# Performance work log

Measured on AMD Instinct MI355X. Metric: run time of the kernel, lower is better.

## Reference

```python
import jax, jax.numpy as jnp
import numpy as np

WS = 7   # window_size
SS = 3   # shift_size
NH = 6   # num_heads
EPS = 1e-5


def _partition(x, ws):
    # [b,h,w,c] -> [b*(h//ws)*(w//ws), ws*ws, c]
    b, h, w, c = x.shape
    x = x.reshape(b, h // ws, ws, w // ws, ws, c)
    return x.transpose(0, 1, 3, 2, 4, 5).reshape(-1, ws * ws, c)


def _reverse(windows, ws, h, w, b):
    c = windows.shape[-1]
    x = windows.reshape(b, h // ws, w // ws, ws, ws, c)
    return x.transpose(0, 1, 3, 2, 4, 5).reshape(b, h, w, c)


def _make_mask(h, w, ws, ss):
    # static (numpy) shifted-window attention mask, [nw, ws*ws, ws*ws]
    img = np.zeros((h, w), dtype=np.float32)
    slices = (slice(0, -ws), slice(-ws, -ss), slice(-ss, None))
    cnt = 0
    for hs in slices:
        for wsl in slices:
            img[hs, wsl] = cnt
            cnt += 1
    mw = img.reshape(h // ws, ws, w // ws, ws).transpose(0, 2, 1, 3).reshape(-1, ws * ws)
    am = mw[:, None, :] - mw[:, :, None]
    mask = np.where(am != 0, -100.0, 0.0).astype(np.float32)
    return jnp.asarray(mask)


def _layernorm(x, g, b):
    mu = jnp.mean(x, axis=-1, keepdims=True)
    var = jnp.var(x, axis=-1, keepdims=True)
    return (x - mu) * jax.lax.rsqrt(var + EPS) * g + b


def setup_inputs() -> dict:
    key = jax.random.key(0)
    ks = jax.random.split(key, 8)
    dim = 192
    s = lambda fan: 1.0 / np.sqrt(fan)
    return {
        "x": jax.random.normal(ks[0], (64, 56, 56, dim), dtype=jnp.float32),
        "n1_g": jnp.ones((dim,), jnp.float32),
        "n1_b": jnp.zeros((dim,), jnp.float32),
        "qkv_w": jax.random.normal(ks[1], (dim, 3 * dim), jnp.float32) * s(dim),
        "qkv_b": jnp.zeros((3 * dim,), jnp.float32),
        "proj_w": jax.random.normal(ks[2], (dim, dim), jnp.float32) * s(dim),
        "proj_b": jnp.zeros((dim,), jnp.float32),
        "n2_g": jnp.ones((dim,), jnp.float32),
        "n2_b": jnp.zeros((dim,), jnp.float32),
        "w1": jax.random.normal(ks[3], (dim, 4 * dim), jnp.float32) * s(dim),
        "b1": jnp.zeros((4 * dim,), jnp.float32),
        "w2": jax.random.normal(ks[4], (4 * dim, dim), jnp.float32) * s(4 * dim),
        "b2": jnp.zeros((dim,), jnp.float32),
    }


def reference(x, n1_g, n1_b, qkv_w, qkv_b, proj_w, proj_b, n2_g, n2_b, w1, b1, w2, b2):
    b, h, w, c = x.shape
    hd = c // NH
    scale = hd ** -0.5

    sc = x
    xn = _layernorm(x, n1_g, n1_b)
    sx = jnp.roll(xn, shift=(-SS, -SS), axis=(1, 2))

    xw = _partition(sx, WS)                      # [B_, n, c], n = WS*WS
    B_, n, _ = xw.shape

    qkv = xw @ qkv_w + qkv_b                      # [B_, n, 3c]
    qkv = qkv.reshape(B_, n, 3, NH, hd).transpose(2, 0, 3, 1, 4)
    q, k, v = qkv[0], qkv[1], qkv[2]              # [B_, NH, n, hd]

    attn = jnp.einsum("whnd,whmd->whnm", q, k) * scale   # [B_, NH, n, n]
    mask = _make_mask(h, w, WS, SS)               # [nw, n, n]
    nw = mask.shape[0]
    attn = attn.reshape(b // nw * 1 if False else b, nw, NH, n, n) if False else attn.reshape(B_ // nw, nw, NH, n, n)
    attn = attn + mask[None, :, None, :, :]
    attn = attn.reshape(-1, NH, n, n)
    attn = jax.nn.softmax(attn, axis=-1)

    out = jnp.einsum("whnm,whmd->whnd", attn, v)  # [B_, NH, n, hd]
    out = out.transpose(0, 2, 1, 3).reshape(B_, n, c)
    out = out @ proj_w + proj_b

    sx = _reverse(out, WS, h, w, b)
    xs = jnp.roll(sx, shift=(SS, SS), axis=(1, 2))

    x2 = sc + xs
    x2n = _layernorm(x2, n2_g, n2_b)
    mlp = jax.nn.gelu(x2n @ w1 + b1, approximate=False) @ w2 + b2
    return x2 + mlp
```

## Files before the change

kernel.cpp:

```cpp
#include <hip/hip_runtime.h>

typedef __attribute__((ext_vector_type(4))) float f32x4;
typedef __attribute__((ext_vector_type(8))) short bf16x8;
typedef __attribute__((ext_vector_type(2))) unsigned int u32x2;

#define NHEAD 6

__device__ __forceinline__ unsigned short f2bf(float f){
  union{float f;unsigned int u;}c; c.f=f;
  unsigned int x=c.u;
  return (unsigned short)((x + 0x7FFFu + ((x>>16)&1u)) >> 16);
}
__device__ __forceinline__ unsigned int cvtpk(float a, float b){
  unsigned int r;
  asm("v_cvt_pk_bf16_f32 %0, %1, %2" : "=v"(r) : "v"(a), "v"(b));
  return r;
}

__global__ void wt_kernel(const float* __restrict__ w, unsigned short* __restrict__ wt,
                          int K, int N){
  int idx = blockIdx.x*256 + threadIdx.x;
  if (idx >= K*N) return;
  int k = idx / N, n = idx - k*N;
  wt[(size_t)n*K + k] = f2bf(w[idx]);
}

template<int SHIFT>
__global__ __launch_bounds__(256) void ln_kernel(const float* __restrict__ x,
    const float* __restrict__ gw, const float* __restrict__ bw,
    unsigned short* __restrict__ out){
  int tok  = blockIdx.x*4 + (threadIdx.x>>6);
  int lane = threadIdx.x & 63;
  const float* row = x + (size_t)tok*192;
  float4 v = make_float4(0.f,0.f,0.f,0.f);
  if (lane < 48) v = *(const float4*)(row + lane*4);
  float s  = v.x+v.y+v.z+v.w;
  float s2 = v.x*v.x+v.y*v.y+v.z*v.z+v.w*v.w;
  #pragma unroll
  for (int off=32; off; off>>=1){ s += __shfl_xor(s,off); s2 += __shfl_xor(s2,off); }
  float mu = s*(1.f/192.f);
  float rs = rsqrtf(s2*(1.f/192.f) - mu*mu + 1e-5f);
  size_t otok;
  if (SHIFT){
    int b = tok/3136; int hw = tok - b*3136; int h = hw/56; int w = hw - h*56;
    int hs = h-3; if (hs<0) hs += 56;
    int wsh = w-3; if (wsh<0) wsh += 56;
    int wr = hs/7, r = hs - wr*7, wc = wsh/7, c = wsh - wc*7;
    otok = ((size_t)b*64 + wr*8 + wc)*49 + r*7 + c;
  } else {
    otok = (size_t)tok;
  }
  if (lane < 48){
    int cb = lane*4;
    float4 g4 = *(const float4*)(gw + cb);
    float4 b4 = *(const float4*)(bw + cb);
    u32x2 o;
    o.x = cvtpk((v.x-mu)*rs*g4.x + b4.x, (v.y-mu)*rs*g4.y + b4.y);
    o.y = cvtpk((v.z-mu)*rs*g4.z + b4.z, (v.w-mu)*rs*g4.w + b4.w);
    *(u32x2*)(out + otok*192 + cb) = o;
  }
}

enum { EPI_QKV=0, EPI_PROJ=1, EPI_GELU=2, EPI_FINAL=3 };

__device__ __forceinline__ float gelu_fast(float v){
  float t = v*(1.59576912f + 0.07135481f*v*v);
  float e = __expf(-t);
  return v/(1.f + e);
}

template<int EPI>
__global__ __launch_bounds__(256) void gemm_kernel(
    const unsigned short* __restrict__ A,
    const unsigned short* __restrict__ BT,
    const float* __restrict__ bias,
    const float* __restrict__ res,
    void* __restrict__ Cout,
    int M, int N, int K)
{
  __shared__ unsigned short lA[128*64];
  __shared__ unsigned short lB[64*64];
  const int tid  = threadIdx.x;
  const int wave = tid>>6, lane = tid&63;
  const int wm = wave>>1, wn = wave&1;
  const int lr = lane&15, lh = lane>>4;

  const int Nb = N>>6;
  int bid = blockIdx.x;
  int yb = bid/(8*Nb); int rr = bid - yb*8*Nb; int xq = rr>>3; int y8 = rr&7;
  const int m0 = (yb*8 + y8)*128, n0 = xq*64;

  f32x4 zero = {0.f,0.f,0.f,0.f};
  f32x4 acc[4][2];
  #pragma unroll
  for (int i=0;i<4;i++){ acc[i][0]=zero; acc[i][1]=zero; }

  const int row8 = tid>>3;
  const int sw   = row8 & 7;
  const int csw  = ((tid&7) ^ sw)*8;
  const unsigned short* Ag = A  + (size_t)(m0 + row8)*K + csw;
  const unsigned short* Bg = BT + (size_t)(n0 + row8)*K + csw;

  for (int kt=0; kt<K; kt+=64){
    __syncthreads();
    #pragma unroll
    for (int i=0;i<4;i++){
      __builtin_amdgcn_global_load_lds(
        (const __attribute__((address_space(1))) void*)(Ag + (size_t)i*32*K + kt),
        (__attribute__((address_space(3))) void*)(lA + (i*256 + wave*64)*8),
        16, 0, 0);
    }
    #pragma unroll
    for (int i=0;i<2;i++){
      __builtin_amdgcn_global_load_lds(
        (const __attribute__((address_space(1))) void*)(Bg + (size_t)i*32*K + kt),
        (__attribute__((address_space(3))) void*)(lB + (i*256 + wave*64)*8),
        16, 0, 0);
    }
    __syncthreads();

    bf16x8 af[4][2], bfv[2][2];
    #pragma unroll
    for (int mi=0;mi<4;mi++)
      #pragma unroll
      for (int ks=0;ks<2;ks++){
        int arow = wm*64+mi*16+lr;
        af[mi][ks] = *(const bf16x8*)&lA[arow*64 + (((ks*4+lh) ^ (lr&7))*8)];
      }
    #pragma unroll
    for (int ni=0;ni<2;ni++)
      #pragma unroll
      for (int ks=0;ks<2;ks++){
        int brow = wn*32+ni*16+lr;
        bfv[ni][ks] = *(const bf16x8*)&lB[brow*64 + (((ks*4+lh) ^ (lr&7))*8)];
      }
    #pragma unroll
    for (int mi=0;mi<4;mi++)
      #pragma unroll
      for (int ni=0;ni<2;ni++)
        #pragma unroll
        for (int ks=0;ks<2;ks++)
          acc[mi][ni] = __builtin_amdgcn_mfma_f32_16x16x32_bf16(
              bfv[ni][ks], af[mi][ks], acc[mi][ni], 0,0,0);
  }

  #pragma unroll
  for (int mi=0;mi<4;mi++){
    const int row = m0 + wm*64 + mi*16 + lr;
    int winr=0, nn=0;
    size_t prow = 0;
    if (EPI == EPI_QKV){
      winr = row/49; nn = row - winr*49;
    } else if (EPI == EPI_PROJ){
      winr = row/49; nn = row - winr*49;
      int b  = winr>>6; int wi = winr&63; int wr_ = wi>>3; int wc_ = wi&7;
      int r7 = nn/7;  int c7 = nn - r7*7;
      int h = wr_*7 + r7 + 3; if (h>=56) h-=56;
      int w = wc_*7 + c7 + 3; if (w>=56) w-=56;
      prow = (((size_t)b*3136) + h*56 + w)*192;
    }
    #pragma unroll
    for (int ni=0;ni<2;ni++){
      const int colb = n0 + wn*32 + ni*16 + lh*4;
      float4 bv4 = *(const float4*)(bias + colb);
      float v0 = acc[mi][ni][0] + bv4.x;
      float v1 = acc[mi][ni][1] + bv4.y;
      float v2 = acc[mi][ni][2] + bv4.z;
      float v3 = acc[mi][ni][3] + bv4.w;
      if (EPI == EPI_QKV){
        int which = colb/192; int rem = colb - which*192;
        int head = rem>>5, d = rem&31;
        size_t idx = (size_t)winr*28224 + (size_t)which*9408 + head*1568 + nn*32 + d;
        u32x2 st; st.x = cvtpk(v0,v1); st.y = cvtpk(v2,v3);
        *(u32x2*)((unsigned short*)Cout + idx) = st;
      } else if (EPI == EPI_GELU){
        u32x2 st; st.x = cvtpk(gelu_fast(v0), gelu_fast(v1));
        st.y = cvtpk(gelu_fast(v2), gelu_fast(v3));
        *(u32x2*)((unsigned short*)Cout + (size_t)row*N + colb) = st;
      } else if (EPI == EPI_FINAL){
        size_t idx = (size_t)row*N + colb;
        float4 rv = *(const float4*)(res + idx);
        float4 o = make_float4(rv.x+v0, rv.y+v1, rv.z+v2, rv.w+v3);
        *(float4*)((float*)Cout + idx) = o;
      } else {
        size_t idx = prow + colb;
        float4 rv = *(const float4*)(res + idx);
        float4 o = make_float4(rv.x+v0, rv.y+v1, rv.z+v2, rv.w+v3);
        *(float4*)((float*)Cout + idx) = o;
      }
    }
  }
}

__global__ __launch_bounds__(256) void attn_kernel(const unsigned short* __restrict__ qkv,
                                                   unsigned short* __restrict__ aout){
  __shared__ __align__(16) unsigned short ldsQK[4][4096];
  __shared__ __align__(16) unsigned short ldsV[4][2048];
  const int wave = threadIdx.x>>6, lane = threadIdx.x&63;
  const int lr = lane&15, lh = lane>>4;
  const int unit = blockIdx.x*4 + wave;
  const int win  = unit/NHEAD, head = unit - win*NHEAD;

  unsigned short* Q  = ldsQK[wave];
  unsigned short* Kl = ldsQK[wave] + 2048;
  unsigned short* P  = ldsQK[wave];
  unsigned short* Vt = ldsV[wave];

  const size_t wbase = (size_t)win*28224 + (size_t)head*1568;
  const unsigned short* gQ = qkv + wbase;
  const unsigned short* gK = qkv + wbase + 9408;
  const unsigned short* gV = qkv + wbase + 18816;

  {
    uint4 z = make_uint4(0,0,0,0);
    #pragma unroll
    for (int i=0;i<4;i++) *(uint4*)&Vt[(i*64+lane)*8] = z;
  }

  #pragma unroll
  for (int i=0;i<4;i++){
    int idx = i*64 + lane;
    if (idx < 196){
      int row = idx>>2, blk = idx&3;
      int sb = (blk ^ (row&3) ^ ((row>>2)&3));
      uint4 dq = *(const uint4*)(gQ + idx*8);
      *(uint4*)&Q[row*32 + sb*8] = dq;
      uint4 dk = *(const uint4*)(gK + idx*8);
      *(uint4*)&Kl[row*32 + sb*8] = dk;
    }
  }
  #pragma unroll
  for (int i=0;i<4;i++){
    int idx = i*64 + lane;
    if (idx < 196){
      int row = idx>>2, d0 = (idx&3)*8;
      uint4 dv = *(const uint4*)(gV + idx*8);
      unsigned int wds[4] = {dv.x, dv.y, dv.z, dv.w};
      int rb = row>>3, re = row&7;
      #pragma unroll
      for (int j=0;j<8;j++){
        unsigned short t = (unsigned short)(wds[j>>1] >> ((j&1)*16));
        Vt[(d0+j)*64 + ((rb ^ j)*8) + re] = t;
      }
    }
  }

  bf16x8 kf[4], qf[4];
  #pragma unroll
  for (int t=0;t<4;t++){
    int row = t*16 + lr;
    int off = row*32 + ((lh ^ (row&3) ^ ((row>>2)&3))*8);
    kf[t] = *(const bf16x8*)&Kl[off];
    qf[t] = *(const bf16x8*)&Q[off];
  }

  f32x4 zero = {0.f,0.f,0.f,0.f};
  f32x4 S[4][4];
  #pragma unroll
  for (int mi=0;mi<4;mi++)
    #pragma unroll
    for (int ni=0;ni<4;ni++)
      S[mi][ni] = __builtin_amdgcn_mfma_f32_16x16x32_bf16(kf[mi], qf[ni], zero, 0,0,0);

  const int wi = win & 63, wr = wi>>3, wc = wi&7;
  const bool hasmask = (wr==7) || (wc==7);
  const float scale = 0.17677669529663687f;

  #pragma unroll
  for (int ni=0;ni<4;ni++){
    int q = ni*16 + lr;
    int idq = 0;
    if (hasmask){
      int qr = q/7, qc = q - qr*7;
      int ih = (wr==7) ? ((qr>=4)?2:1) : 0;
      int iw = (wc==7) ? ((qc>=4)?2:1) : 0;
      idq = ih*3 + iw;
    }
    #pragma unroll
    for (int mi=0;mi<4;mi++){
      #pragma unroll
      for (int r=0;r<4;r++){
        int key = mi*16 + lh*4 + r;
        float s;
        if (key >= 49) s = -1e30f;
        else {
          float add = 0.f;
          if (hasmask){
            int kr = key/7, kc = key - kr*7;
            int ih = (wr==7) ? ((kr>=4)?2:1) : 0;
            int iw = (wc==7) ? ((kc>=4)?2:1) : 0;
            add = ((ih*3+iw) == idq) ? 0.f : -100.f;
          }
          s = S[mi][ni][r]*scale + add;
        }
        S[mi][ni][r] = s;
      }
    }
    float m = -1e30f;
    #pragma unroll
    for (int mi=0;mi<4;mi++)
      #pragma unroll
      for (int r=0;r<4;r++) m = fmaxf(m, S[mi][ni][r]);
    m = fmaxf(m, __shfl_xor(m, 16));
    m = fmaxf(m, __shfl_xor(m, 32));
    float sum = 0.f;
    #pragma unroll
    for (int mi=0;mi<4;mi++)
      #pragma unroll
      for (int r=0;r<4;r++){
        float p = __expf(S[mi][ni][r] - m);
        S[mi][ni][r] = p; sum += p;
      }
    sum += __shfl_xor(sum, 16);
    sum += __shfl_xor(sum, 32);
    float inv = 1.f/sum;
    #pragma unroll
    for (int mi=0;mi<4;mi++){
      int keyb = mi*16 + lh*4;
      int blk = keyb>>3, e0 = keyb&7;
      int addr = q*64 + ((blk ^ (q&7))*8) + e0;
      *(unsigned int*)&P[addr]   = cvtpk(S[mi][ni][0]*inv, S[mi][ni][1]*inv);
      *(unsigned int*)&P[addr+2] = cvtpk(S[mi][ni][2]*inv, S[mi][ni][3]*inv);
    }
  }

  bf16x8 vf[2][2];
  #pragma unroll
  for (int mt=0;mt<2;mt++)
    #pragma unroll
    for (int ks=0;ks<2;ks++){
      int row = mt*16 + lr;
      vf[mt][ks] = *(const bf16x8*)&Vt[row*64 + (((ks*4+lh) ^ (row&7))*8)];
    }
  f32x4 O[2][4];
  #pragma unroll
  for (int ni=0;ni<4;ni++){
    int q = ni*16 + lr;
    bf16x8 pf0 = *(const bf16x8*)&P[q*64 + (((0*4+lh) ^ (q&7))*8)];
    bf16x8 pf1 = *(const bf16x8*)&P[q*64 + (((1*4+lh) ^ (q&7))*8)];
    #pragma unroll
    for (int mt=0;mt<2;mt++){
      f32x4 t = __builtin_amdgcn_mfma_f32_16x16x32_bf16(vf[mt][0], pf0, zero, 0,0,0);
      O[mt][ni] = __builtin_amdgcn_mfma_f32_16x16x32_bf16(vf[mt][1], pf1, t, 0,0,0);
    }
  }

  #pragma unroll
  for (int ni=0;ni<4;ni++){
    int q = ni*16 + lr;
    if (q < 49){
      size_t ob = ((size_t)win*49 + q)*192 + head*32 + lh*4;
      #pragma unroll
      for (int mt=0;mt<2;mt++){
        u32x2 st;
        st.x = cvtpk(O[mt][ni][0], O[mt][ni][1]);
        st.y = cvtpk(O[mt][ni][2], O[mt][ni][3]);
        *(u32x2*)(aout + ob + mt*16) = st;
      }
    }
  }
}

extern "C" void kernel_launch(void* const* d_in, const int* in_sizes, int n_in,
                              void* d_out, int out_size, void* d_ws, size_t ws_size,
                              hipStream_t stream){
  (void)in_sizes; (void)n_in; (void)out_size; (void)ws_size;
  const float* x      = (const float*)d_in[0];
  const float* n1_g   = (const float*)d_in[1];
  const float* n1_b   = (const float*)d_in[2];
  const float* qkv_w  = (const float*)d_in[3];
  const float* qkv_b  = (const float*)d_in[4];
  const float* proj_w = (const float*)d_in[5];
  const float* proj_b = (const float*)d_in[6];
  const float* n2_g   = (const float*)d_in[7];
  const float* n2_b   = (const float*)d_in[8];
  const float* w1     = (const float*)d_in[9];
  const float* b1     = (const float*)d_in[10];
  const float* w2     = (const float*)d_in[11];
  const float* b2     = (const float*)d_in[12];

  char* ws = (char*)d_ws;
  unsigned short* qkvT = (unsigned short*)(ws + 0);
  unsigned short* projT= (unsigned short*)(ws + 221184);
  unsigned short* w1T  = (unsigned short*)(ws + 294912);
  unsigned short* w2T  = (unsigned short*)(ws + 589824);
  unsigned short* bufA = (unsigned short*)(ws + 884736);
  unsigned short* bufB = (unsigned short*)(ws + 77955072);
  float*          x2   = (float*)        (ws + 386236416);
  float* out = (float*)d_out;
  const int M = 200704;

  wt_kernel<<<432,256,0,stream>>>(qkv_w, qkvT, 192, 576);
  wt_kernel<<<144,256,0,stream>>>(proj_w, projT, 192, 192);
  wt_kernel<<<576,256,0,stream>>>(w1,    w1T,  192, 768);
  wt_kernel<<<576,256,0,stream>>>(w2,    w2T,  768, 192);

  ln_kernel<1><<<50176,256,0,stream>>>(x, n1_g, n1_b, bufA);
  gemm_kernel<EPI_QKV  ><<< 9*1568, 256,0,stream>>>(bufA, qkvT, qkv_b, nullptr, bufB, M, 576, 192);
  attn_kernel<<<6144,256,0,stream>>>(bufB, bufA);
  gemm_kernel<EPI_PROJ ><<< 3*1568, 256,0,stream>>>(bufA, projT, proj_b, x, x2, M, 192, 192);
  ln_kernel<0><<<50176,256,0,stream>>>(x2, n2_g, n2_b, bufA);
  gemm_kernel<EPI_GELU ><<<12*1568, 256,0,stream>>>(bufA, w1T, b1, nullptr, bufB, M, 768, 192);
  gemm_kernel<EPI_FINAL><<< 3*1568, 256,0,stream>>>(bufB, w2T, b2, x2, out, M, 192, 768);
}
```

Measured before the change: 740.4 us.

## Add persistent B-resident GEMM with double-buffered A tiles for K=192 GEMMs

Adds a new GEMM kernel for the K=192 matmuls (QKV, proj, MLP fc1). Each block loads its full 64x192 weight slice into LDS once and keeps the B fragments in registers. It then walks 7 consecutive 128-row M tiles, double-buffering A loads across k-chunks and tiles. This is meant to cut redundant weight reloads and per-block launch overhead, and to overlap global loads with MFMA work. In exchange it uses more LDS and registers per block (launch_bounds 256,2) and launches fewer blocks, and the old gemm_kernel is reduced to the final-residual epilogue only.

```diff
diff --git a/kernel.cpp b/kernel.cpp
--- a/kernel.cpp
+++ b/kernel.cpp
@@ -67,6 +67,161 @@
   float t = v*(1.59576912f + 0.07135481f*v*v);
   float e = __expf(-t);
   return v/(1.f + e);
+}
+
+template<int EPI>
+__global__ __launch_bounds__(256,2) void gemm_bres(
+    const unsigned short* __restrict__ A,
+    const unsigned short* __restrict__ BT,
+    const float* __restrict__ bias,
+    const float* __restrict__ res,
+    void* __restrict__ Cout,
+    int M, int N, int TM, int Nb)
+{
+  const int K = 192;
+  __shared__ unsigned short lB[64*192];
+  __shared__ unsigned short lA[2][128*64];
+  const int tid  = threadIdx.x;
+  const int wave = tid>>6, lane = tid&63;
+  const int wm = wave>>1, wn = wave&1;
+  const int lr = lane&15, lh = lane>>4;
+
+  int bid = blockIdx.x;
+  int y8 = bid&7; int u = bid>>3; int x = u % Nb; int yb = u / Nb;
+  const int y  = yb*8 + y8;
+  const int n0 = x*64;
+
+  {
+    #pragma unroll
+    for (int p=0;p<6;p++){
+      int chunkid = p*256 + tid;
+      int col = chunkid/24, cp = chunkid - col*24;
+      int cs = (cp & 0x18) | ((cp&7) ^ (col&7));
+      __builtin_amdgcn_global_load_lds(
+        (const __attribute__((address_space(1))) void*)(BT + (size_t)(n0+col)*K + cs*8),
+        (__attribute__((address_space(3))) void*)(lB + p*2048 + wave*512),
+        16, 0, 0);
+    }
+  }
+  const int row8 = tid>>3;
+  const int csw  = ((tid&7) ^ (row8&7))*8;
+  const unsigned short* Ag = A + ((size_t)y*TM*128 + row8)*K + csw;
+  #pragma unroll
+  for (int i=0;i<4;i++){
+    __builtin_amdgcn_global_load_lds(
+      (const __attribute__((address_space(1))) void*)(Ag + (size_t)i*32*K),
+      (__attribute__((address_space(3))) void*)(lA[0] + i*2048 + wave*512),
+      16, 0, 0);
+  }
+  __syncthreads();
+
+  bf16x8 bfv[3][2][2];
+  #pragma unroll
+  for (int kc=0;kc<3;kc++)
+    #pragma unroll
+    for (int ni=0;ni<2;ni++)
+      #pragma unroll
+      for (int ks=0;ks<2;ks++){
+        int col = wn*32 + ni*16 + lr;
+        int pc  = kc*8 + ((ks*4+lh) ^ (lr&7));
+        bfv[kc][ni][ks] = *(const bf16x8*)&lB[col*192 + pc*8];
+      }
+
+  f32x4 zero = {0.f,0.f,0.f,0.f};
+  f32x4 acc[4][2];
+  #pragma unroll
+  for (int i=0;i<4;i++){ acc[i][0]=zero; acc[i][1]=zero; }
+
+  int buf = 0;
+  int mrow = y*TM*128;
+
+  for (int mloc=0; mloc<TM; ++mloc){
+    #pragma unroll
+    for (int kc=0; kc<3; ++kc){
+      if (kc < 2){
+        #pragma unroll
+        for (int i=0;i<4;i++){
+          __builtin_amdgcn_global_load_lds(
+            (const __attribute__((address_space(1))) void*)(Ag + (size_t)i*32*K + (kc+1)*64),
+            (__attribute__((address_space(3))) void*)(lA[buf^1] + i*2048 + wave*512),
+            16, 0, 0);
+        }
+      } else if (mloc < TM-1){
+        #pragma unroll
+        for (int i=0;i<4;i++){
+          __builtin_amdgcn_global_load_lds(
+            (const __attribute__((address_space(1))) void*)(Ag + (size_t)(128 + i*32)*K),
+            (__attribute__((address_space(3))) void*)(lA[buf^1] + i*2048 + wave*512),
+            16, 0, 0);
+        }
+      }
+      bf16x8 af[4][2];
+      #pragma unroll
+      for (int mi=0;mi<4;mi++)
+        #pragma unroll
+        for (int ks=0;ks<2;ks++){
+          int arow = wm*64+mi*16+lr;
+          af[mi][ks] = *(const bf16x8*)&lA[buf][arow*64 + (((ks*4+lh) ^ (lr&7))*8)];
+        }
+      #pragma unroll
+      for (int mi=0;mi<4;mi++)
+        #pragma unroll
+        for (int ni=0;ni<2;ni++)
+          #pragma unroll
+          for (int ks=0;ks<2;ks++)
+            acc[mi][ni] = __builtin_amdgcn_mfma_f32_16x16x32_bf16(
+                bfv[kc][ni][ks], af[mi][ks], acc[mi][ni], 0,0,0);
+
+      if (kc == 2){
+        #pragma unroll
+        for (int mi=0;mi<4;mi++){
+          const int row = mrow + wm*64 + mi*16 + lr;
+          int winr=0, nn=0;
+          size_t prow = 0;
+          if (EPI == EPI_QKV){
+            winr = row/49; nn = row - winr*49;
+          } else if (EPI == EPI_PROJ){
+            winr = row/49; nn = row - winr*49;
+            int b  = winr>>6; int wi = winr&63; int wr_ = wi>>3; int wc_ = wi&7;
+            int r7 = nn/7;  int c7 = nn - r7*7;
+            int h = wr_*7 + r7 + 3; if (h>=56) h-=56;
+            int w = wc_*7 + c7 + 3; if (w>=56) w-=56;
+            prow = (((size_t)b*3136) + h*56 + w)*192;
+          }
+          #pragma unroll
+          for (int ni=0;ni<2;ni++){
+            const int colb = n0 + wn*32 + ni*16 + lh*4;
+            float4 bv4 = *(const float4*)(bias + colb);
+            float v0 = acc[mi][ni][0] + bv4.x;
+            float v1 = acc[mi][ni][1] + bv4.y;
+            float v2 = acc[mi][ni][2] + bv4.z;
+            float v3 = acc[mi][ni][3] + bv4.w;
+            if (EPI == EPI_QKV){
+              int which = colb/192; int rem = colb - which*192;
+              int head = rem>>5, d = rem&31;
+              size_t idx = (size_t)winr*28224 + (size_t)which*9408 + head*1568 + nn*32 + d;
+              u32x2 st; st.x = cvtpk(v0,v1); st.y = cvtpk(v2,v3);
+              *(u32x2*)((unsigned short*)Cout + idx) = st;
+            } else if (EPI == EPI_GELU){
+              u32x2 st; st.x = cvtpk(gelu_fast(v0), gelu_fast(v1));
+              st.y = cvtpk(gelu_fast(v2), gelu_fast(v3));
+              *(u32x2*)((unsigned short*)Cout + (size_t)row*N + colb) = st;
+            } else {
+              size_t idx = prow + colb;
+              float4 rv = *(const float4*)(res + idx);
+              float4 o = make_float4(rv.x+v0, rv.y+v1, rv.z+v2, rv.w+v3);
+              *(float4*)((float*)Cout + idx) = o;
+            }
+            acc[mi][ni] = zero;
+          }
+        }
+      }
+      __syncthreads();
+      buf ^= 1;
+    }
+    Ag += (size_t)128*K;
+    mrow += 128;
+  }
 }
 
 template<int EPI>
@@ -96,8 +251,7 @@
   for (int i=0;i<4;i++){ acc[i][0]=zero; acc[i][1]=zero; }
 
   const int row8 = tid>>3;
-  const int sw   = row8 & 7;
-  const int csw  = ((tid&7) ^ sw)*8;
+  const int csw  = ((tid&7) ^ (row8&7))*8;
   const unsigned short* Ag = A  + (size_t)(m0 + row8)*K + csw;
   const unsigned short* Bg = BT + (size_t)(n0 + row8)*K + csw;
 
@@ -147,18 +301,6 @@
   #pragma unroll
   for (int mi=0;mi<4;mi++){
     const int row = m0 + wm*64 + mi*16 + lr;
-    int winr=0, nn=0;
-    size_t prow = 0;
-    if (EPI == EPI_QKV){
-      winr = row/49; nn = row - winr*49;
-    } else if (EPI == EPI_PROJ){
-      winr = row/49; nn = row - winr*49;
-      int b  = winr>>6; int wi = winr&63; int wr_ = wi>>3; int wc_ = wi&7;
-      int r7 = nn/7;  int c7 = nn - r7*7;
-      int h = wr_*7 + r7 + 3; if (h>=56) h-=56;
-      int w = wc_*7 + c7 + 3; if (w>=56) w-=56;
-      prow = (((size_t)b*3136) + h*56 + w)*192;
-    }
     #pragma unroll
     for (int ni=0;ni<2;ni++){
       const int colb = n0 + wn*32 + ni*16 + lh*4;
@@ -167,27 +309,10 @@
       float v1 = acc[mi][ni][1] + bv4.y;
       float v2 = acc[mi][ni][2] + bv4.z;
       float v3 = acc[mi][ni][3] + bv4.w;
-      if (EPI == EPI_QKV){
-        int which = colb/192; int rem = colb - which*192;
-        int head = rem>>5, d = rem&31;
-        size_t idx = (size_t)winr*28224 + (size_t)which*9408 + head*1568 + nn*32 + d;
-        u32x2 st; st.x = cvtpk(v0,v1); st.y = cvtpk(v2,v3);
-        *(u32x2*)((unsigned short*)Cout + idx) = st;
-      } else if (EPI == EPI_GELU){
-        u32x2 st; st.x = cvtpk(gelu_fast(v0), gelu_fast(v1));
-        st.y = cvtpk(gelu_fast(v2), gelu_fast(v3));
-        *(u32x2*)((unsigned short*)Cout + (size_t)row*N + colb) = st;
-      } else if (EPI == EPI_FINAL){
-        size_t idx = (size_t)row*N + colb;
-        float4 rv = *(const float4*)(res + idx);
-        float4 o = make_float4(rv.x+v0, rv.y+v1, rv.z+v2, rv.w+v3);
-        *(float4*)((float*)Cout + idx) = o;
-      } else {
-        size_t idx = prow + colb;
-        float4 rv = *(const float4*)(res + idx);
-        float4 o = make_float4(rv.x+v0, rv.y+v1, rv.z+v2, rv.w+v3);
-        *(float4*)((float*)Cout + idx) = o;
-      }
+      size_t idx = (size_t)row*N + colb;
+      float4 rv = *(const float4*)(res + idx);
+      float4 o = make_float4(rv.x+v0, rv.y+v1, rv.z+v2, rv.w+v3);
+      *(float4*)((float*)Cout + idx) = o;
     }
   }
 }
@@ -389,6 +514,7 @@
   float*          x2   = (float*)        (ws + 386236416);
   float* out = (float*)d_out;
   const int M = 200704;
+  const int TM = 7;
 
   wt_kernel<<<432,256,0,stream>>>(qkv_w, qkvT, 192, 576);
   wt_kernel<<<144,256,0,stream>>>(proj_w, projT, 192, 192);
@@ -396,10 +522,10 @@
   wt_kernel<<<576,256,0,stream>>>(w2,    w2T,  768, 192);
 
   ln_kernel<1><<<50176,256,0,stream>>>(x, n1_g, n1_b, bufA);
-  gemm_kernel<EPI_QKV  ><<< 9*1568, 256,0,stream>>>(bufA, qkvT, qkv_b, nullptr, bufB, M, 576, 192);
+  gemm_bres<EPI_QKV  ><<< 9*224, 256,0,stream>>>(bufA, qkvT, qkv_b, nullptr, bufB, M, 576, TM, 9);
   attn_kernel<<<6144,256,0,stream>>>(bufB, bufA);
-  gemm_kernel<EPI_PROJ ><<< 3*1568, 256,0,stream>>>(bufA, projT, proj_b, x, x2, M, 192, 192);
+  gemm_bres<EPI_PROJ ><<< 3*224, 256,0,stream>>>(bufA, projT, proj_b, x, x2, M, 192, TM, 3);
   ln_kernel<0><<<50176,256,0,stream>>>(x2, n2_g, n2_b, bufA);
-  gemm_kernel<EPI_GELU ><<<12*1568, 256,0,stream>>>(bufA, w1T, b1, nullptr, bufB, M, 768, 192);
+  gemm_bres<EPI_GELU ><<<12*224, 256,0,stream>>>(bufA, w1T, b1, nullptr, bufB, M, 768, TM, 12);
   gemm_kernel<EPI_FINAL><<< 3*1568, 256,0,stream>>>(bufB, w2T, b2, x2, out, M, 192, 768);
 }
```

Measured after the change: 778.0 us. +5.1%, slower.

## Add 128x128 GEMM tile kernel with 64-wide remainder kernel

Applied to the files above, without the earlier changes.

Adds a GEMM variant that computes 128x128 output tiles, so each wave does 4x4 MFMA accumulators, and keeps a 64-column variant for leftover column strips. Each GEMM is split into a 128-wide launch plus a 64-wide remainder launch where N is not a multiple of 128. The goal is more reuse of each A tile loaded into shared memory and fewer total blocks and global A reads. In exchange each thread holds more accumulator registers, which may lower occupancy, and the extra kernel launches add some overhead.

```diff
diff --git a/kernel.cpp b/kernel.cpp
--- a/kernel.cpp
+++ b/kernel.cpp
@@ -70,13 +70,148 @@
 }
 
 template<int EPI>
-__global__ __launch_bounds__(256) void gemm_kernel(
+__device__ __forceinline__ void epi_store(void* Cout, const float* bias,
+    const float* res, int N, int row, int colb, f32x4 a,
+    int winr, int nn, size_t prow){
+  float4 bv4 = *(const float4*)(bias + colb);
+  float v0 = a[0] + bv4.x;
+  float v1 = a[1] + bv4.y;
+  float v2 = a[2] + bv4.z;
+  float v3 = a[3] + bv4.w;
+  if (EPI == EPI_QKV){
+    int which = colb/192; int rem = colb - which*192;
+    int head = rem>>5, d = rem&31;
+    size_t idx = (size_t)winr*28224 + (size_t)which*9408 + head*1568 + nn*32 + d;
+    u32x2 st; st.x = cvtpk(v0,v1); st.y = cvtpk(v2,v3);
+    *(u32x2*)((unsigned short*)Cout + idx) = st;
+  } else if (EPI == EPI_GELU){
+    u32x2 st; st.x = cvtpk(gelu_fast(v0), gelu_fast(v1));
+    st.y = cvtpk(gelu_fast(v2), gelu_fast(v3));
+    *(u32x2*)((unsigned short*)Cout + (size_t)row*N + colb) = st;
+  } else if (EPI == EPI_FINAL){
+    size_t idx = (size_t)row*N + colb;
+    float4 rv = *(const float4*)(res + idx);
+    float4 o = make_float4(rv.x+v0, rv.y+v1, rv.z+v2, rv.w+v3);
+    *(float4*)((float*)Cout + idx) = o;
+  } else {
+    size_t idx = prow + colb;
+    float4 rv = *(const float4*)(res + idx);
+    float4 o = make_float4(rv.x+v0, rv.y+v1, rv.z+v2, rv.w+v3);
+    *(float4*)((float*)Cout + idx) = o;
+  }
+}
+
+template<int EPI>
+__device__ __forceinline__ void epi_rowidx(int row, int& winr, int& nn, size_t& prow){
+  winr=0; nn=0; prow=0;
+  if (EPI == EPI_QKV){
+    winr = row/49; nn = row - winr*49;
+  } else if (EPI == EPI_PROJ){
+    winr = row/49; nn = row - winr*49;
+    int b  = winr>>6; int wi = winr&63; int wr_ = wi>>3; int wc_ = wi&7;
+    int r7 = nn/7;  int c7 = nn - r7*7;
+    int h = wr_*7 + r7 + 3; if (h>=56) h-=56;
+    int w = wc_*7 + c7 + 3; if (w>=56) w-=56;
+    prow = (((size_t)b*3136) + h*56 + w)*192;
+  }
+}
+
+template<int EPI>
+__global__ __launch_bounds__(256) void gemm128(
     const unsigned short* __restrict__ A,
     const unsigned short* __restrict__ BT,
     const float* __restrict__ bias,
     const float* __restrict__ res,
     void* __restrict__ Cout,
-    int M, int N, int K)
+    int M, int N, int Nb, int K)
+{
+  __shared__ unsigned short lA[128*64];
+  __shared__ unsigned short lB[128*64];
+  const int tid  = threadIdx.x;
+  const int wave = tid>>6, lane = tid&63;
+  const int wm = wave>>1, wn = wave&1;
+  const int lr = lane&15, lh = lane>>4;
+
+  int bid = blockIdx.x;
+  int yb = bid/(8*Nb); int rr = bid - yb*8*Nb; int xq = rr>>3; int y8 = rr&7;
+  const int m0 = (yb*8 + y8)*128, n0 = xq*128;
+
+  f32x4 zero = {0.f,0.f,0.f,0.f};
+  f32x4 acc[4][4];
+  #pragma unroll
+  for (int i=0;i<4;i++)
+    #pragma unroll
+    for (int j=0;j<4;j++) acc[i][j]=zero;
+
+  const int row8 = tid>>3;
+  const int csw  = ((tid&7) ^ (row8&7))*8;
+  const unsigned short* Ag = A  + (size_t)(m0 + row8)*K + csw;
+  const unsigned short* Bg = BT + (size_t)(n0 + row8)*K + csw;
+
+  for (int kt=0; kt<K; kt+=64){
+    __syncthreads();
+    #pragma unroll
+    for (int i=0;i<4;i++){
+      __builtin_amdgcn_global_load_lds(
+        (const __attribute__((address_space(1))) void*)(Ag + (size_t)i*32*K + kt),
+        (__attribute__((address_space(3))) void*)(lA + (i*256 + wave*64)*8),
+        16, 0, 0);
+    }
+    #pragma unroll
+    for (int i=0;i<4;i++){
+      __builtin_amdgcn_global_load_lds(
+        (const __attribute__((address_space(1))) void*)(Bg + (size_t)i*32*K + kt),
+        (__attribute__((address_space(3))) void*)(lB + (i*256 + wave*64)*8),
+        16, 0, 0);
+    }
+    __syncthreads();
+
+    bf16x8 af[4][2], bfv[4][2];
+    #pragma unroll
+    for (int mi=0;mi<4;mi++)
+      #pragma unroll
+      for (int ks=0;ks<2;ks++){
+        int arow = wm*64+mi*16+lr;
+        af[mi][ks] = *(const bf16x8*)&lA[arow*64 + (((ks*4+lh) ^ (lr&7))*8)];
+      }
+    #pragma unroll
+    for (int ni=0;ni<4;ni++)
+      #pragma unroll
+      for (int ks=0;ks<2;ks++){
+        int brow = wn*64+ni*16+lr;
+        bfv[ni][ks] = *(const bf16x8*)&lB[brow*64 + (((ks*4+lh) ^ (lr&7))*8)];
+      }
+    #pragma unroll
+    for (int mi=0;mi<4;mi++)
+      #pragma unroll
+      for (int ni=0;ni<4;ni++)
+        #pragma unroll
+        for (int ks=0;ks<2;ks++)
+          acc[mi][ni] = __builtin_amdgcn_mfma_f32_16x16x32_bf16(
+              bfv[ni][ks], af[mi][ks], acc[mi][ni], 0,0,0);
+  }
+
+  #pragma unroll
+  for (int mi=0;mi<4;mi++){
+    const int row = m0 + wm*64 + mi*16 + lr;
+    int winr, nn; size_t prow;
+    epi_rowidx<EPI>(row, winr, nn, prow);
+    #pragma unroll
+    for (int ni=0;ni<4;ni++){
+      const int colb = n0 + wn*64 + ni*16 + lh*4;
+      epi_store<EPI>(Cout, bias, res, N, row, colb, acc[mi][ni], winr, nn, prow);
+    }
+  }
+}
+
+template<int EPI>
+__global__ __launch_bounds__(256) void gemm64(
+    const unsigned short* __restrict__ A,
+    const unsigned short* __restrict__ BT,
+    const float* __restrict__ bias,
+    const float* __restrict__ res,
+    void* __restrict__ Cout,
+    int M, int N, int K, int n_off, int Nb)
 {
   __shared__ unsigned short lA[128*64];
   __shared__ unsigned short lB[64*64];
@@ -85,10 +220,9 @@
   const int wm = wave>>1, wn = wave&1;
   const int lr = lane&15, lh = lane>>4;
 
-  const int Nb = N>>6;
   int bid = blockIdx.x;
   int yb = bid/(8*Nb); int rr = bid - yb*8*Nb; int xq = rr>>3; int y8 = rr&7;
-  const int m0 = (yb*8 + y8)*128, n0 = xq*64;
+  const int m0 = (yb*8 + y8)*128, n0 = n_off + xq*64;
 
   f32x4 zero = {0.f,0.f,0.f,0.f};
   f32x4 acc[4][2];
@@ -96,8 +230,7 @@
   for (int i=0;i<4;i++){ acc[i][0]=zero; acc[i][1]=zero; }
 
   const int row8 = tid>>3;
-  const int sw   = row8 & 7;
-  const int csw  = ((tid&7) ^ sw)*8;
+  const int csw  = ((tid&7) ^ (row8&7))*8;
   const unsigned short* Ag = A  + (size_t)(m0 + row8)*K + csw;
   const unsigned short* Bg = BT + (size_t)(n0 + row8)*K + csw;
 
@@ -147,47 +280,12 @@
   #pragma unroll
   for (int mi=0;mi<4;mi++){
     const int row = m0 + wm*64 + mi*16 + lr;
-    int winr=0, nn=0;
-    size_t prow = 0;
-    if (EPI == EPI_QKV){
-      winr = row/49; nn = row - winr*49;
-    } else if (EPI == EPI_PROJ){
-      winr = row/49; nn = row - winr*49;
-      int b  = winr>>6; int wi = winr&63; int wr_ = wi>>3; int wc_ = wi&7;
-      int r7 = nn/7;  int c7 = nn - r7*7;
-      int h = wr_*7 + r7 + 3; if (h>=56) h-=56;
-      int w = wc_*7 + c7 + 3; if (w>=56) w-=56;
-      prow = (((size_t)b*3136) + h*56 + w)*192;
-    }
+    int winr, nn; size_t prow;
+    epi_rowidx<EPI>(row, winr, nn, prow);
     #pragma unroll
     for (int ni=0;ni<2;ni++){
       const int colb = n0 + wn*32 + ni*16 + lh*4;
-      float4 bv4 = *(const float4*)(bias + colb);
-      float v0 = acc[mi][ni][0] + bv4.x;
-      float v1 = acc[mi][ni][1] + bv4.y;
-      float v2 = acc[mi][ni][2] + bv4.z;
-      float v3 = acc[mi][ni][3] + bv4.w;
-      if (EPI == EPI_QKV){
-        int which = colb/192; int rem = colb - which*192;
-        int head = rem>>5, d = rem&31;
-        size_t idx = (size_t)winr*28224 + (size_t)which*9408 + head*1568 + nn*32 + d;
-        u32x2 st; st.x = cvtpk(v0,v1); st.y = cvtpk(v2,v3);
-        *(u32x2*)((unsigned short*)Cout + idx) = st;
-      } else if (EPI == EPI_GELU){
-        u32x2 st; st.x = cvtpk(gelu_fast(v0), gelu_fast(v1));
-        st.y = cvtpk(gelu_fast(v2), gelu_fast(v3));
-        *(u32x2*)((unsigned short*)Cout + (size_t)row*N + colb) = st;
-      } else if (EPI == EPI_FINAL){
-        size_t idx = (size_t)row*N + colb;
-        float4 rv = *(const float4*)(res + idx);
-        float4 o = make_float4(rv.x+v0, rv.y+v1, rv.z+v2, rv.w+v3);
-        *(float4*)((float*)Cout + idx) = o;
-      } else {
-        size_t idx = prow + colb;
-        float4 rv = *(const float4*)(res + idx);
-        float4 o = make_float4(rv.x+v0, rv.y+v1, rv.z+v2, rv.w+v3);
-        *(float4*)((float*)Cout + idx) = o;
-      }
+      epi_store<EPI>(Cout, bias, res, N, row, colb, acc[mi][ni], winr, nn, prow);
     }
   }
 }
@@ -396,10 +494,19 @@
   wt_kernel<<<576,256,0,stream>>>(w2,    w2T,  768, 192);
 
   ln_kernel<1><<<50176,256,0,stream>>>(x, n1_g, n1_b, bufA);
-  gemm_kernel<EPI_QKV  ><<< 9*1568, 256,0,stream>>>(bufA, qkvT, qkv_b, nullptr, bufB, M, 576, 192);
+
+  gemm128<EPI_QKV ><<<4*1568, 256,0,stream>>>(bufA, qkvT, qkv_b, nullptr, bufB, M, 576, 4, 192);
+  gemm64 <EPI_QKV ><<<1*1568, 256,0,stream>>>(bufA, qkvT, qkv_b, nullptr, bufB, M, 576, 192, 512, 1);
+
   attn_kernel<<<6144,256,0,stream>>>(bufB, bufA);
-  gemm_kernel<EPI_PROJ ><<< 3*1568, 256,0,stream>>>(bufA, projT, proj_b, x, x2, M, 192, 192);
+
+  gemm128<EPI_PROJ><<<1*1568, 256,0,stream>>>(bufA, projT, proj_b, x, x2, M, 192, 1, 192);
+  gemm64 <EPI_PROJ><<<1*1568, 256,0,stream>>>(bufA, projT, proj_b, x, x2, M, 192, 192, 128, 1);
+
   ln_kernel<0><<<50176,256,0,stream>>>(x2, n2_g, n2_b, bufA);
-  gemm_kernel<EPI_GELU ><<<12*1568, 256,0,stream>>>(bufA, w1T, b1, nullptr, bufB, M, 768, 192);
-  gemm_kernel<EPI_FINAL><<< 3*1568, 256,0,stream>>>(bufB, w2T, b2, x2, out, M, 192, 768);
-}
+
+  gemm128<EPI_GELU><<<6*1568, 256,0,stream>>>(bufA, w1T, b1, nullptr, bufB, M, 768, 6, 192);
+
+  gemm128<EPI_FINAL><<<1*1568, 256,0,stream>>>(bufB, w2T, b2, x2, out, M, 192, 1, 768);
+  gemm64 <EPI_FINAL><<<1*1568, 256,0,stream>>>(bufB, w2T, b2, x2, out, M, 192, 768, 128, 1);
+}
```

Measured after the change: 835.7 us. +12.9%, slower.
